# Optimization experiments

Measured on AMD Instinct MI355X. Metric: run time of the kernel, lower is better.

## Reference

```python
import jax, jax.numpy as jnp
import numpy as np

NUM_CLASSES = 2047
TIME_WEIGHT = 2.0
EOS_COEF = 0.1
B, Q, N = 64, 100, 16


def _lsa(cost):
    """Jonker-Volgenant min-cost assignment for rectangular cost [R, C], R <= C.
    Returns (row_ind, col_ind) with row_ind = arange(R). Equivalent to
    scipy.optimize.linear_sum_assignment."""
    R, Cn = cost.shape
    u = np.zeros(R + 1)
    v = np.zeros(Cn + 1)
    p = np.zeros(Cn + 1, dtype=np.int64)  # p[j] = 1-based row matched to col j (0 = free)
    for i in range(1, R + 1):
        p[0] = i
        j0 = 0
        minv = np.full(Cn + 1, np.inf)
        used = np.zeros(Cn + 1, dtype=bool)
        way = np.zeros(Cn + 1, dtype=np.int64)
        while True:
            used[j0] = True
            i0 = p[j0]
            cur = cost[i0 - 1] - u[i0] - v[1:]
            free = ~used[1:]
            upd = free & (cur < minv[1:])
            minv[1:] = np.where(upd, cur, minv[1:])
            way[1:] = np.where(upd, j0, way[1:])
            j1 = int(np.argmin(np.where(free, minv[1:], np.inf))) + 1
            delta = minv[j1]
            u[p[used]] += delta
            v[used] -= delta
            minv[1:] = np.where(free, minv[1:] - delta, minv[1:])
            j0 = j1
            if p[j0] == 0:
                break
        while j0 != 0:  # augment along the alternating path
            j1 = way[j0]
            p[j0] = p[j1]
            j0 = j1
    col4row = np.zeros(R, dtype=np.int64)
    for j in range(1, Cn + 1):
        if p[j] > 0:
            col4row[p[j] - 1] = j - 1
    return np.arange(R), col4row


def _match(C):
    """C: np.ndarray [B, Q, N]. Returns (query_idx [B,N], target_idx [B,N])."""
    b, q, n = C.shape
    qs = np.zeros((b, n), np.int64)
    ts = np.zeros((b, n), np.int64)
    for i in range(b):
        r, c = _lsa(C[i].T)  # rows = targets (N), cols = queries (Q); N <= Q
        ts[i] = r
        qs[i] = c
    return qs, ts


def setup_inputs() -> dict:
    key = jax.random.key(0)
    k1, k2, k3, k4 = jax.random.split(key, 4)
    pred_logits = jax.random.normal(k1, (B, Q, NUM_CLASSES + 1), dtype=jnp.float32)
    pred_time = jax.random.uniform(k2, (B, Q, 1), dtype=jnp.float32)
    labels = jax.random.randint(k3, (B, N), 1, NUM_CLASSES + 1)  # class 0 = no-object
    timestamps = jax.random.uniform(k4, (B, N, 1), dtype=jnp.float32)
    return {"pred_logits": pred_logits, "pred_time": pred_time,
            "labels": labels, "timestamps": timestamps}


def reference(pred_logits, pred_time, labels, timestamps):
    b, q = pred_logits.shape[:2]
    n = labels.shape[1]
    # --- Hungarian matching cost (detached, host-side assignment as in the original) ---
    probs = jax.nn.softmax(pred_logits, axis=-1)                              # [B,Q,C+1]
    cost_class = -jnp.take_along_axis(probs, labels[:, None, :], axis=2)      # [B,Q,N]
    cost_time = jnp.abs(pred_time[..., 0][:, :, None] -
                        timestamps[..., 0][:, None, :])                       # [B,Q,N] (cdist p=1)
    C = cost_class + TIME_WEIGHT * cost_time
    Cnp = np.nan_to_num(np.asarray(jax.device_get(C)),
                        nan=100.0, posinf=100.0, neginf=-100.0)
    qs, ts = _match(Cnp)
    qs_j = jnp.asarray(qs)  # matched query indices  [B,N]
    ts_j = jnp.asarray(ts)  # matched target indices [B,N]
    # --- weighted cross entropy over all queries ---
    class_ids = jnp.take_along_axis(labels, ts_j, axis=1)                     # [B,N]
    batch_ar = jnp.arange(b)[:, None]
    target_classes = jnp.zeros((b, q), dtype=jnp.int64).at[batch_ar, qs_j].set(class_ids)
    logZ = jax.nn.logsumexp(pred_logits, axis=-1)                             # [B,Q]
    tgt_logit = jnp.take_along_axis(pred_logits, target_classes[..., None], axis=2)[..., 0]
    nll = logZ - tgt_logit                                                    # [B,Q]
    ce_w = jnp.ones(NUM_CLASSES + 1, jnp.float32).at[0].set(EOS_COEF)
    w = ce_w[target_classes]
    loss_ce = jnp.sum(w * nll) / jnp.sum(w)
    # --- L1 loss on matched timestamps ---
    matched_pred = pred_time[batch_ar, qs_j, 0]                               # [B,N]
    matched_tgt = jnp.take_along_axis(timestamps[..., 0], ts_j, axis=1)       # [B,N]
    loss_time = jnp.mean(jnp.abs(matched_pred - matched_tgt))
    return loss_ce + TIME_WEIGHT * loss_time
```

## Files before the change

### kernel.cpp

```cpp
#include <hip/hip_runtime.h>
#include <hip/hip_bf16.h>
#include <math.h>

#define BB 64
#define QQ 100
#define NN 16
#define CC 2048
#define TIME_WEIGHT 2.0f
#define EOS_COEF 0.1f

__device__ __forceinline__ double readlane_d(double x, int lane) {
    int lo = __builtin_amdgcn_readlane(__double2loint(x), lane);
    int hi = __builtin_amdgcn_readlane(__double2hiint(x), lane);
    return __hiloint2double(hi, lo);
}

__global__ __launch_bounds__(256) void lse_cost_kernel(
    const float* __restrict__ logits, const float* __restrict__ ptime,
    const int* __restrict__ labels, const float* __restrict__ tstamp,
    float* __restrict__ logZ, float* __restrict__ CgT,
    float* __restrict__ lsepart, float* __restrict__ sums, int* __restrict__ counter)
{
    if (blockIdx.x == 0 && threadIdx.x == 0) {
        sums[0] = 0.f; sums[1] = 0.f; *counter = 0;
    }
    const int wave = threadIdx.x >> 6;
    const int lane = threadIdx.x & 63;
    const int bq = blockIdx.x * 4 + wave;
    const int b = bq / QQ;
    const float4* row4 = (const float4*)(logits + (size_t)bq * CC);

    float4 v[8];
    #pragma unroll
    for (int c = 0; c < 8; ++c) v[c] = row4[c * 64 + lane];

    const float pt = ptime[bq];
    int lab = 0; float ts = 0.f;
    if (lane < NN) {
        lab = labels[b * NN + lane];
        ts  = tstamp[b * NN + lane];
    }

    float m = -INFINITY;
    #pragma unroll
    for (int c = 0; c < 8; ++c)
        m = fmaxf(m, fmaxf(fmaxf(v[c].x, v[c].y), fmaxf(v[c].z, v[c].w)));
    #pragma unroll
    for (int s = 1; s < 64; s <<= 1) m = fmaxf(m, __shfl_xor(m, s, 64));

    float sum = 0.f;
    #pragma unroll
    for (int c = 0; c < 8; ++c)
        sum += expf(v[c].x - m) + expf(v[c].y - m) +
               expf(v[c].z - m) + expf(v[c].w - m);
    #pragma unroll
    for (int s = 1; s < 64; s <<= 1) sum += __shfl_xor(sum, s, 64);

    const float lz = m + logf(sum);
    if (lane == 0) logZ[bq] = lz;

    if (lane < NN) {
        float lg = logits[(size_t)bq * CC + lab];
        float cc = -expf(lg - lz);
        float ct = fabsf(pt - ts);
        float val = cc + TIME_WEIGHT * ct;
        if (isnan(val)) val = 100.0f;
        else if (isinf(val)) val = (val > 0.f) ? 100.0f : -100.0f;
        CgT[(size_t)bq * NN + lane] = val;
    }

    __shared__ float red[4];
    if (lane == 0) red[wave] = lz - logits[(size_t)bq * CC];
    __syncthreads();
    if (threadIdx.x == 0)
        lsepart[blockIdx.x] = red[0] + red[1] + red[2] + red[3];
}

__global__ __launch_bounds__(64) void hungarian_kernel(
    const float* __restrict__ CgT, const float* __restrict__ logits,
    const float* __restrict__ ptime, const int* __restrict__ labels,
    const float* __restrict__ tstamp, const float* __restrict__ logZ,
    const float* __restrict__ lsepart, float* __restrict__ sums,
    int* __restrict__ counter, float* __restrict__ out)
{
    const int b = blockIdx.x;
    const int t = threadIdx.x;

    __shared__ int qsl[NN];

    const int jc0 = t + 1;
    const int jc1 = t + 65;
    const bool has2 = (jc1 <= QQ);
    const int t2 = has2 ? (t + 64) : t;

    const float* colbase = CgT + (size_t)b * QQ * NN;
    const float4* cp0 = (const float4*)(colbase + t * NN);
    const float4* cp1 = (const float4*)(colbase + t2 * NN);
    const float4 a0 = cp0[0], a1 = cp0[1], a2 = cp0[2], a3 = cp0[3];
    const float4 b0 = cp1[0], b1 = cp1[1], b2 = cp1[2], b3 = cp1[3];

    double v0 = 0.0, v1 = 0.0;
    double ureg = 0.0;
    int preg0 = 0, preg1 = 0;
    const double INF = __builtin_inf();

    for (int i = 1; i <= NN; ++i) {
        double minv0 = INF, minv1 = INF;
        bool used0 = false, used1 = false;
        int way0 = 0, way1 = 0;
        bool inTree = (t == i - 1);
        int j0 = 0;
        int i0 = i;

        while (true) {
            used0 |= (j0 == jc0);
            used1 |= (j0 == jc1);
            inTree = inTree || (t == i0 - 1);
            const double u_i0 = readlane_d(ureg, i0 - 1);

            const int mrow = i0 - 1;
            float4 ha = (mrow & 8) ? ((mrow & 4) ? a3 : a2)
                                   : ((mrow & 4) ? a1 : a0);
            float4 hb = (mrow & 8) ? ((mrow & 4) ? b3 : b2)
                                   : ((mrow & 4) ? b1 : b0);
            float ca = (mrow & 2) ? ((mrow & 1) ? ha.w : ha.z)
                                  : ((mrow & 1) ? ha.y : ha.x);
            float cb = (mrow & 2) ? ((mrow & 1) ? hb.w : hb.z)
                                  : ((mrow & 1) ? hb.y : hb.x);

            if (!used0) {
                double cur = (double)ca - u_i0 - v0;
                if (cur < minv0) { minv0 = cur; way0 = j0; }
            }
            if (has2 && !used1) {
                double cur = (double)cb - u_i0 - v1;
                if (cur < minv1) { minv1 = cur; way1 = j0; }
            }

            double m0 = used0 ? INF : minv0;
            double m1 = (has2 && !used1) ? minv1 : INF;
            double gmin = fmin(m0, m1);
            #pragma unroll
            for (int s = 1; s < 16; s <<= 1)
                gmin = fmin(gmin, __shfl_xor(gmin, s, 64));
            {
                double h0 = readlane_d(gmin, 0);
                double h1 = readlane_d(gmin, 16);
                double h2 = readlane_d(gmin, 32);
                double h3 = readlane_d(gmin, 48);
                gmin = fmin(fmin(h0, h1), fmin(h2, h3));
            }
            unsigned long long A  = __ballot(!used0 && (minv0 == gmin));
            unsigned long long Bm = __ballot(has2 && !used1 && (minv1 == gmin));
            int j1 = (A != 0ull) ? ((int)__builtin_ctzll(A) + 1)
                                 : ((int)__builtin_ctzll(Bm) + 65);
            const double delta = gmin;

            if (inTree) ureg += delta;
            if (used0) v0 -= delta; else minv0 -= delta;
            if (has2) { if (used1) v1 -= delta; else minv1 -= delta; }

            j0 = j1;
            int pj = (j0 <= 64) ? __builtin_amdgcn_readlane(preg0, j0 - 1)
                                : __builtin_amdgcn_readlane(preg1, j0 - 65);
            if (pj == 0) break;
            i0 = pj;
        }

        while (j0 != 0) {
            int jn = (j0 <= 64) ? __builtin_amdgcn_readlane(way0, j0 - 1)
                                : __builtin_amdgcn_readlane(way1, j0 - 65);
            int pv;
            if (jn == 0) pv = i;
            else pv = (jn <= 64) ? __builtin_amdgcn_readlane(preg0, jn - 1)
                                 : __builtin_amdgcn_readlane(preg1, jn - 65);
            if (j0 == jc0) preg0 = pv;
            if (has2 && j0 == jc1) preg1 = pv;
            j0 = jn;
        }
    }

    if (preg0 > 0) qsl[preg0 - 1] = jc0 - 1;
    if (has2 && preg1 > 0) qsl[preg1 - 1] = jc1 - 1;
    __syncthreads();

    float corr = 0.f, tl = 0.f;
    if (t < NN) {
        int qcol = qsl[t];
        int lab = labels[b * NN + t];
        int bq = b * QQ + qcol;
        float lz = logZ[bq];
        float lgm = logits[(size_t)bq * CC + lab];
        float lg0 = logits[(size_t)bq * CC];
        corr = (lz - lgm) - EOS_COEF * (lz - lg0);
        tl = fabsf(ptime[bq] - tstamp[b * NN + t]);
    }
    #pragma unroll
    for (int s = 1; s < 64; s <<= 1) {
        corr += __shfl_xor(corr, s, 64);
        tl   += __shfl_xor(tl, s, 64);
    }

    int old = 0;
    if (t == 0) {
        atomicAdd(&sums[0], corr);
        atomicAdd(&sums[1], tl);
        __threadfence();
        old = atomicAdd(counter, 1);
    }
    old = __shfl(old, 0, 64);
    if (old == BB - 1) {
        __threadfence();
        float r0 = 0.f;
        #pragma unroll
        for (int k = 0; k < 25; ++k) r0 += lsepart[t + 64 * k];
        #pragma unroll
        for (int s = 1; s < 64; s <<= 1) r0 += __shfl_xor(r0, s, 64);
        if (t == 0) {
            float s0 = atomicAdd(&sums[0], 0.0f);
            float s1 = atomicAdd(&sums[1], 0.0f);
            const float sum_w = (float)(BB * NN) * 1.0f
                              + (float)(BB * (QQ - NN)) * EOS_COEF;
            float loss_ce = (EOS_COEF * r0 + s0) / sum_w;
            float loss_t  = s1 / (float)(BB * NN);
            out[0] = loss_ce + TIME_WEIGHT * loss_t;
        }
    }
}

extern "C" void kernel_launch(void* const* d_in, const int* in_sizes, int n_in,
                              void* d_out, int out_size, void* d_ws, size_t ws_size,
                              hipStream_t stream) {
    const float* logits = (const float*)d_in[0];
    const float* ptime  = (const float*)d_in[1];
    const int*   labels = (const int*)d_in[2];
    const float* tstamp = (const float*)d_in[3];
    float* out = (float*)d_out;

    char* ws = (char*)d_ws;
    float* logZ    = (float*)ws;
    float* CgT     = (float*)(ws + 25600);
    float* lsepart = (float*)(ws + 435200);
    float* sums    = (float*)(ws + 441600);
    int*   counter = (int*)(ws + 441608);

    lse_cost_kernel<<<1600, 256, 0, stream>>>(logits, ptime, labels, tstamp,
                                              logZ, CgT, lsepart, sums, counter);
    hungarian_kernel<<<BB, 64, 0, stream>>>(CgT, logits, ptime, labels, tstamp,
                                            logZ, lsepart, sums, counter, out);
}
```

Baseline: 115.9 us.

## Use fp32 Hungarian solver with shuffle-based min reduction and two rows per wave

The Hungarian assignment kernel switches its dual variables and min tracking from double to float, and replaces the xor-butterfly plus readlane min reduction with an 8-way shuffle gather followed by 8 readlanes. The log-sum-exp kernel now processes two rows per wave with half as many blocks, and reuses the already loaded logit for the class-0 term. The intent is to shorten the serial latency of the assignment loop and raise memory-level parallelism in the LSE pass. Float duals can break ties differently from the double-precision reference, which may produce a different matching when costs are near-equal.

```diff
diff --git a/kernel.cpp b/kernel.cpp
--- a/kernel.cpp
+++ b/kernel.cpp
@@ -9,10 +9,8 @@
 #define TIME_WEIGHT 2.0f
 #define EOS_COEF 0.1f
 
-__device__ __forceinline__ double readlane_d(double x, int lane) {
-    int lo = __builtin_amdgcn_readlane(__double2loint(x), lane);
-    int hi = __builtin_amdgcn_readlane(__double2hiint(x), lane);
-    return __hiloint2double(hi, lo);
+__device__ __forceinline__ float readlane_f(float x, int lane) {
+    return __int_as_float(__builtin_amdgcn_readlane(__float_as_int(x), lane));
 }
 
 __global__ __launch_bounds__(256) void lse_cost_kernel(
@@ -26,54 +24,74 @@
     }
     const int wave = threadIdx.x >> 6;
     const int lane = threadIdx.x & 63;
-    const int bq = blockIdx.x * 4 + wave;
-    const int b = bq / QQ;
-    const float4* row4 = (const float4*)(logits + (size_t)bq * CC);
-
-    float4 v[8];
-    #pragma unroll
-    for (int c = 0; c < 8; ++c) v[c] = row4[c * 64 + lane];
-
-    const float pt = ptime[bq];
-    int lab = 0; float ts = 0.f;
-    if (lane < NN) {
-        lab = labels[b * NN + lane];
-        ts  = tstamp[b * NN + lane];
-    }
-
-    float m = -INFINITY;
-    #pragma unroll
-    for (int c = 0; c < 8; ++c)
-        m = fmaxf(m, fmaxf(fmaxf(v[c].x, v[c].y), fmaxf(v[c].z, v[c].w)));
-    #pragma unroll
-    for (int s = 1; s < 64; s <<= 1) m = fmaxf(m, __shfl_xor(m, s, 64));
-
-    float sum = 0.f;
-    #pragma unroll
-    for (int c = 0; c < 8; ++c)
-        sum += expf(v[c].x - m) + expf(v[c].y - m) +
-               expf(v[c].z - m) + expf(v[c].w - m);
-    #pragma unroll
-    for (int s = 1; s < 64; s <<= 1) sum += __shfl_xor(sum, s, 64);
-
-    const float lz = m + logf(sum);
-    if (lane == 0) logZ[bq] = lz;
-
-    if (lane < NN) {
+    const int bqA = blockIdx.x * 8 + wave * 2;
+    const int bqB = bqA + 1;
+    const float4* rowA = (const float4*)(logits + (size_t)bqA * CC);
+    const float4* rowB = (const float4*)(logits + (size_t)bqB * CC);
+
+    float4 va[8], vb[8];
+    #pragma unroll
+    for (int c = 0; c < 8; ++c) { va[c] = rowA[c * 64 + lane]; vb[c] = rowB[c * 64 + lane]; }
+
+    float ma = -INFINITY, mb = -INFINITY;
+    #pragma unroll
+    for (int c = 0; c < 8; ++c) {
+        ma = fmaxf(ma, fmaxf(fmaxf(va[c].x, va[c].y), fmaxf(va[c].z, va[c].w)));
+        mb = fmaxf(mb, fmaxf(fmaxf(vb[c].x, vb[c].y), fmaxf(vb[c].z, vb[c].w)));
+    }
+    #pragma unroll
+    for (int s = 1; s < 64; s <<= 1) {
+        ma = fmaxf(ma, __shfl_xor(ma, s, 64));
+        mb = fmaxf(mb, __shfl_xor(mb, s, 64));
+    }
+
+    float sa = 0.f, sb = 0.f;
+    #pragma unroll
+    for (int c = 0; c < 8; ++c) {
+        sa += expf(va[c].x - ma) + expf(va[c].y - ma) +
+              expf(va[c].z - ma) + expf(va[c].w - ma);
+        sb += expf(vb[c].x - mb) + expf(vb[c].y - mb) +
+              expf(vb[c].z - mb) + expf(vb[c].w - mb);
+    }
+    #pragma unroll
+    for (int s = 1; s < 64; s <<= 1) {
+        sa += __shfl_xor(sa, s, 64);
+        sb += __shfl_xor(sb, s, 64);
+    }
+
+    const float lzA = ma + logf(sa);
+    const float lzB = mb + logf(sb);
+    if (lane == 0) { logZ[bqA] = lzA; logZ[bqB] = lzB; }
+
+    if (lane < 32) {
+        const int n = lane & 15;
+        const int bq = (lane < 16) ? bqA : bqB;
+        const float lz = (lane < 16) ? lzA : lzB;
+        const int b = bq / QQ;
+        int lab = labels[b * NN + n];
+        float ts = tstamp[b * NN + n];
+        float pt = ptime[bq];
         float lg = logits[(size_t)bq * CC + lab];
         float cc = -expf(lg - lz);
         float ct = fabsf(pt - ts);
         float val = cc + TIME_WEIGHT * ct;
         if (isnan(val)) val = 100.0f;
         else if (isinf(val)) val = (val > 0.f) ? 100.0f : -100.0f;
-        CgT[(size_t)bq * NN + lane] = val;
-    }
-
-    __shared__ float red[4];
-    if (lane == 0) red[wave] = lz - logits[(size_t)bq * CC];
+        CgT[(size_t)bq * NN + n] = val;
+    }
+
+    __shared__ float red[8];
+    if (lane == 0) {
+        red[wave * 2]     = lzA - va[0].x;
+        red[wave * 2 + 1] = lzB - vb[0].x;
+    }
     __syncthreads();
-    if (threadIdx.x == 0)
-        lsepart[blockIdx.x] = red[0] + red[1] + red[2] + red[3];
+    if (threadIdx.x == 0) {
+        float r = 0.f;
+        #pragma unroll
+        for (int k = 0; k < 8; ++k) r += red[k];
+        lsepart[blockIdx.x] = r;
+    }
 }
 
 __global__ __launch_bounds__(64) void hungarian_kernel(
@@ -99,13 +117,14 @@
     const float4 a0 = cp0[0], a1 = cp0[1], a2 = cp0[2], a3 = cp0[3];
     const float4 b0 = cp1[0], b1 = cp1[1], b2 = cp1[2], b3 = cp1[3];
 
-    double v0 = 0.0, v1 = 0.0;
-    double ureg = 0.0;
+    float v0 = 0.f, v1 = 0.f;
+    float ureg = 0.f;
     int preg0 = 0, preg1 = 0;
-    const double INF = __builtin_inf();
+    const float INF = __builtin_inff();
+    const int gbase = (t & 7) << 3;
 
     for (int i = 1; i <= NN; ++i) {
-        double minv0 = INF, minv1 = INF;
+        float minv0 = INF, minv1 = INF;
         bool used0 = false, used1 = false;
         int way0 = 0, way1 = 0;
         bool inTree = (t == i - 1);
@@ -116,7 +135,7 @@
             used0 |= (j0 == jc0);
             used1 |= (j0 == jc1);
             inTree = inTree || (t == i0 - 1);
-            const double u_i0 = readlane_d(ureg, i0 - 1);
+            const float u_i0 = readlane_f(ureg, i0 - 1);
 
             const int mrow = i0 - 1;
             float4 ha = (mrow & 8) ? ((mrow & 4) ? a3 : a2)
@@ -129,32 +148,44 @@
                                   : ((mrow & 1) ? hb.y : hb.x);
 
             if (!used0) {
-                double cur = (double)ca - u_i0 - v0;
+                float cur = ca - u_i0 - v0;
                 if (cur < minv0) { minv0 = cur; way0 = j0; }
             }
             if (has2 && !used1) {
-                double cur = (double)cb - u_i0 - v1;
+                float cur = cb - u_i0 - v1;
                 if (cur < minv1) { minv1 = cur; way1 = j0; }
             }
 
-            double m0 = used0 ? INF : minv0;
-            double m1 = (has2 && !used1) ? minv1 : INF;
-            double gmin = fmin(m0, m1);
-            #pragma unroll
-            for (int s = 1; s < 16; s <<= 1)
-                gmin = fmin(gmin, __shfl_xor(gmin, s, 64));
-            {
-                double h0 = readlane_d(gmin, 0);
-                double h1 = readlane_d(gmin, 16);
-                double h2 = readlane_d(gmin, 32);
-                double h3 = readlane_d(gmin, 48);
-                gmin = fmin(fmin(h0, h1), fmin(h2, h3));
-            }
+            float m0 = used0 ? INF : minv0;
+            float m1 = (has2 && !used1) ? minv1 : INF;
+            float mm = fminf(m0, m1);
+
+            float g0 = __shfl(mm, gbase + 0, 64);
+            float g1 = __shfl(mm, gbase + 1, 64);
+            float g2 = __shfl(mm, gbase + 2, 64);
+            float g3 = __shfl(mm, gbase + 3, 64);
+            float g4 = __shfl(mm, gbase + 4, 64);
+            float g5 = __shfl(mm, gbase + 5, 64);
+            float g6 = __shfl(mm, gbase + 6, 64);
+            float g7 = __shfl(mm, gbase + 7, 64);
+            float cmin = fminf(fminf(fminf(g0, g1), fminf(g2, g3)),
+                               fminf(fminf(g4, g5), fminf(g6, g7)));
+            float h0 = readlane_f(cmin, 0);
+            float h1 = readlane_f(cmin, 1);
+            float h2 = readlane_f(cmin, 2);
+            float h3 = readlane_f(cmin, 3);
+            float h4 = readlane_f(cmin, 4);
+            float h5 = readlane_f(cmin, 5);
+            float h6 = readlane_f(cmin, 6);
+            float h7 = readlane_f(cmin, 7);
+            float gmin = fminf(fminf(fminf(h0, h1), fminf(h2, h3)),
+                               fminf(fminf(h4, h5), fminf(h6, h7)));
+
             unsigned long long A  = __ballot(!used0 && (minv0 == gmin));
             unsigned long long Bm = __ballot(has2 && !used1 && (minv1 == gmin));
             int j1 = (A != 0ull) ? ((int)__builtin_ctzll(A) + 1)
                                  : ((int)__builtin_ctzll(Bm) + 65);
-            const double delta = gmin;
+            const float delta = gmin;
 
             if (inTree) ureg += delta;
             if (used0) v0 -= delta; else minv0 -= delta;
@@ -213,7 +244,10 @@
         __threadfence();
         float r0 = 0.f;
         #pragma unroll
-        for (int k = 0; k < 25; ++k) r0 += lsepart[t + 64 * k];
+        for (int k = 0; k < 13; ++k) {
+            int idx = t + 64 * k;
+            if (idx < 800) r0 += lsepart[idx];
+        }
         #pragma unroll
         for (int s = 1; s < 64; s <<= 1) r0 += __shfl_xor(r0, s, 64);
         if (t == 0) {
@@ -241,11 +275,11 @@
     float* logZ    = (float*)ws;
     float* CgT     = (float*)(ws + 25600);
     float* lsepart = (float*)(ws + 435200);
-    float* sums    = (float*)(ws + 441600);
-    int*   counter = (int*)(ws + 441608);
-
-    lse_cost_kernel<<<1600, 256, 0, stream>>>(logits, ptime, labels, tstamp,
-                                              logZ, CgT, lsepart, sums, counter);
+    float* sums    = (float*)(ws + 438400);
+    int*   counter = (int*)(ws + 438408);
+
+    lse_cost_kernel<<<800, 256, 0, stream>>>(logits, ptime, labels, tstamp,
+                                             logZ, CgT, lsepart, sums, counter);
     hungarian_kernel<<<BB, 64, 0, stream>>>(CgT, logits, ptime, labels, tstamp,
                                             logZ, lsepart, sums, counter, out);
 }
```

After: 113.3 us. 1.02x faster.
